# Optimization experiments

Hardware: AMD Instinct MI355X
Metric: run time of the kernel (lower is better)

## Reference

```python
import jax, jax.numpy as jnp
import numpy as np

SEQ_LEN, BATCH, INPUT, HIDDEN, OUTPUT = 2048, 64, 256, 256, 256


def setup_inputs() -> dict:
    key = jax.random.key(0)
    ks = jax.random.split(key, 6)
    return {
        "x": jax.random.normal(ks[0], (SEQ_LEN, BATCH, INPUT), dtype=jnp.float32),
        "h0": jax.random.normal(ks[1], (BATCH, HIDDEN), dtype=jnp.float32),
        "i2h_weight": jax.random.normal(ks[2], (INPUT + HIDDEN, HIDDEN), dtype=jnp.float32) * 0.05,
        "i2h_bias": jax.random.normal(ks[3], (HIDDEN,), dtype=jnp.float32) * 0.05,
        "h2o_weight": jax.random.normal(ks[4], (HIDDEN, OUTPUT), dtype=jnp.float32) * 0.05,
        "h2o_bias": jax.random.normal(ks[5], (OUTPUT,), dtype=jnp.float32) * 0.05,
    }


def reference(x, h0, i2h_weight, i2h_bias, h2o_weight, h2o_bias):
    # Vanilla RNN: per timestep t:
    #   h = tanh(concat(x_t, h) @ W_i2h + b_i2h)
    #   y_t = h @ W_h2o + b_h2o
    # Split W_i2h into input/hidden blocks so the concat is expressed as two GEMMs.
    w_xh = i2h_weight[:x.shape[-1]]   # [input, hidden]
    w_hh = i2h_weight[x.shape[-1]:]   # [hidden, hidden]

    def step(h, x_t):
        h_new = jnp.tanh(x_t @ w_xh + h @ w_hh + i2h_bias)  # [batch, hidden]
        y_t = h_new @ h2o_weight + h2o_bias                  # [batch, output]
        return h_new, y_t

    _, outputs = jax.lax.scan(step, h0, x)  # outputs: [seq, batch, output]
    return outputs
```

## Files before the change

### kernel.cpp

```cpp
#include <hip/hip_runtime.h>
#include <cstdint>
#include <cstddef>

typedef __attribute__((ext_vector_type(8))) short short8;
typedef __attribute__((ext_vector_type(4))) float f32x4;
typedef __attribute__((ext_vector_type(2))) float f32x2;
typedef __attribute__((ext_vector_type(2))) unsigned int u32x2;

#define SEQ 2048
#define NB  64
#define HID 256
#define M_TOTAL (SEQ*NB)

__device__ __forceinline__ unsigned short f2bf(float x){
  unsigned u = __float_as_uint(x);
  u += 0x7fffu + ((u>>16)&1u);
  return (unsigned short)(u>>16);
}

__global__ void k_convert_x(const float* __restrict__ x, unsigned short* __restrict__ xb){
  size_t i = (size_t)blockIdx.x*256 + threadIdx.x;
  f32x4 v = ((const f32x4*)x)[i];
  unsigned a0=f2bf(v[0]), a1=f2bf(v[1]), a2=f2bf(v[2]), a3=f2bf(v[3]);
  u32x2 o; o[0] = a0 | (a1<<16); o[1] = a2 | (a3<<16);
  ((u32x2*)xb)[i] = o;
}

__global__ void k_convert_w(const float* __restrict__ i2h, const float* __restrict__ h2o,
                            unsigned short* __restrict__ BT1, unsigned short* __restrict__ BT3){
  int k = blockIdx.x; int n = threadIdx.x;
  BT1[n*256+k] = f2bf(i2h[k*256+n]);
  BT3[n*256+k] = f2bf(h2o[k*256+n]);
}

__global__ __launch_bounds__(256) void k_gemm(
    const unsigned short* __restrict__ A, const unsigned short* __restrict__ BT,
    const float* __restrict__ bias, float* __restrict__ C)
{
  __shared__ __align__(16) unsigned short As[128*64];
  __shared__ __align__(16) unsigned short Bs[128*64];
  int tid = threadIdx.x;
  int bm = blockIdx.x, bn = blockIdx.y;
  int l = tid & 63, wv = tid >> 6;
  int wm = wv >> 1, wn = wv & 1;
  int lr = l & 15, lq = l >> 4;

  f32x4 acc[4][4];
  #pragma unroll
  for (int i=0;i<4;i++)
    #pragma unroll
    for (int j=0;j<4;j++) acc[i][j] = (f32x4)0.f;

  for (int kb=0; kb<4; ++kb){
    int k0 = kb*64;
    #pragma unroll
    for (int it=0; it<4; ++it){
      int f = it*256 + tid;
      int m = f >> 3;
      int kk = (f & 7) * 8;
      short8 va = *(const short8*)(A  + (size_t)(bm*128+m)*256 + k0 + kk);
      short8 vb = *(const short8*)(BT + (size_t)(bn*128+m)*256 + k0 + kk);
      *(short8*)(As + m*64 + kk) = va;
      *(short8*)(Bs + m*64 + kk) = vb;
    }
    __syncthreads();
    #pragma unroll
    for (int kt=0; kt<2; ++kt){
      short8 af[4], bfr[4];
      #pragma unroll
      for (int mt=0;mt<4;mt++){
        int row = wm*64 + mt*16 + lr;
        af[mt] = *(const short8*)(As + row*64 + kt*32 + lq*8);
      }
      #pragma unroll
      for (int nt=0;nt<4;nt++){
        int row = wn*64 + nt*16 + lr;
        bfr[nt] = *(const short8*)(Bs + row*64 + kt*32 + lq*8);
      }
      #pragma unroll
      for (int mt=0;mt<4;mt++)
        #pragma unroll
        for (int nt=0;nt<4;nt++)
          acc[mt][nt] = __builtin_amdgcn_mfma_f32_16x16x32_bf16(af[mt], bfr[nt], acc[mt][nt], 0, 0, 0);
    }
    __syncthreads();
  }
  #pragma unroll
  for (int nt=0;nt<4;nt++){
    int gn = bn*128 + wn*64 + nt*16 + lr;
    float bv = bias[gn];
    #pragma unroll
    for (int mt=0;mt<4;mt++){
      int gm = bm*128 + wm*64 + mt*16 + lq*4;
      #pragma unroll
      for (int r=0;r<4;r++)
        C[(size_t)(gm+r)*256 + gn] = acc[mt][nt][r] + bv;
    }
  }
}

__global__ __launch_bounds__(1024, 4) void k_scan(
    const float* __restrict__ i2h,
    const float* __restrict__ h0,
    const float* __restrict__ pre,
    unsigned short* __restrict__ H)
{
  __shared__ __align__(16) float hbuf[256];
  __shared__ __align__(16) float red[16*256];
  int b   = blockIdx.x;
  int tid = threadIdx.x;
  int jg  = tid & 63;
  int kc  = tid >> 6;

  f32x4 w[16];
  const float* Wp = i2h + (size_t)(256 + kc*16)*256 + jg*4;
  #pragma unroll
  for (int i=0;i<16;i++)
    w[i] = *(const f32x4*)(Wp + (size_t)i*256);

  if (tid < 256) hbuf[tid] = h0[b*256 + tid];

  float pv = 0.f, p1 = 0.f;
  if (tid < 256){
    pv = pre[(size_t)b*256 + tid];
    p1 = pre[((size_t)1*NB + b)*256 + tid];
  }
  __syncthreads();

  float* myred = red + kc*256 + jg*4;

  for (int t=0; t<SEQ; ++t){
    const f32x4* hp = (const f32x4*)(hbuf + kc*16);
    f32x4 acc = (f32x4)0.f;
    #pragma unroll
    for (int i=0;i<4;i++){
      f32x4 h4 = hp[i];
      acc += h4[0]*w[4*i+0];
      acc += h4[1]*w[4*i+1];
      acc += h4[2]*w[4*i+2];
      acc += h4[3]*w[4*i+3];
    }
    *(f32x4*)myred = acc;
    __syncthreads();

    if (tid < 256){
      float p2 = (t+2 < SEQ) ? pre[((size_t)(t+2)*NB + b)*256 + tid] : 0.f;
      float s = pv;
      #pragma unroll
      for (int k2=0;k2<16;k2++) s += red[k2*256 + tid];
      float e = __expf(2.f*s);
      float h = 1.f - 2.f/(e+1.f);
      hbuf[tid] = h;
      H[((size_t)t*NB + b)*256 + tid] = f2bf(h);
      pv = p1; p1 = p2;
    }
    __syncthreads();
  }
}

extern "C" void kernel_launch(void* const* d_in, const int* in_sizes, int n_in,
                              void* d_out, int out_size, void* d_ws, size_t ws_size,
                              hipStream_t stream) {
  const float* x     = (const float*)d_in[0];
  const float* h0    = (const float*)d_in[1];
  const float* i2h   = (const float*)d_in[2];
  const float* i2h_b = (const float*)d_in[3];
  const float* h2o   = (const float*)d_in[4];
  const float* h2o_b = (const float*)d_in[5];
  float* out = (float*)d_out;

  unsigned short* xb  = (unsigned short*)d_ws;
  unsigned short* BT1 = (unsigned short*)((char*)d_ws + (size_t)M_TOTAL*HID*2);
  unsigned short* BT3 = BT1 + 256*256;

  k_convert_x<<<M_TOTAL*HID/(256*4), 256, 0, stream>>>(x, xb);
  k_convert_w<<<256, 256, 0, stream>>>(i2h, h2o, BT1, BT3);

  dim3 g1(M_TOTAL/128, 2);
  k_gemm<<<g1, 256, 0, stream>>>(xb, BT1, i2h_b, out);
  k_scan<<<NB, 1024, 0, stream>>>(i2h, h0, out, xb);
  k_gemm<<<g1, 256, 0, stream>>>(xb, BT3, h2o_b, out);
}
```

Before: 1.654 ms.

## Reduce scan partial sums with DPP lane rotations and lighter barriers

New measurement: 1.965 ms. 18.8% more time.

```diff
diff --git a/kernel.cpp b/kernel.cpp
--- a/kernel.cpp
+++ b/kernel.cpp
@@ -16,6 +16,12 @@
   unsigned u = __float_as_uint(x);
   u += 0x7fffu + ((u>>16)&1u);
   return (unsigned short)(u>>16);
+}
+
+template<int CTRL>
+__device__ __forceinline__ float dpp_rot(float x){
+  return __int_as_float(__builtin_amdgcn_update_dpp(
+      0, __float_as_int(x), CTRL, 0xF, 0xF, true));
 }
 
 __global__ void k_convert_x(const float* __restrict__ x, unsigned short* __restrict__ xb){
@@ -106,55 +112,81 @@
     unsigned short* __restrict__ H)
 {
   __shared__ __align__(16) float hbuf[256];
-  __shared__ __align__(16) float red[16*256];
-  int b   = blockIdx.x;
-  int tid = threadIdx.x;
-  int jg  = tid & 63;
-  int kc  = tid >> 6;
-
-  f32x4 w[16];
-  const float* Wp = i2h + (size_t)(256 + kc*16)*256 + jg*4;
+  __shared__ __align__(16) float red[4*256];
+  const int b   = blockIdx.x;
+  const int tid = threadIdx.x;
+  const int l   = tid & 63;
+  const int wv  = tid >> 6;
+  const int ks  = wv & 3;
+  const int kc  = l & 3;
+  const int j0  = (wv >> 2)*64 + (l >> 2)*4;
+
+  f32x4 wr[16];
+  {
+    const float* Wb = i2h + (size_t)256*256 + ((size_t)(ks*64 + kc*16))*256 + j0;
+    #pragma unroll
+    for (int m=0;m<16;m++) wr[m] = *(const f32x4*)(Wb + (size_t)m*256);
+  }
   #pragma unroll
-  for (int i=0;i<16;i++)
-    w[i] = *(const f32x4*)(Wp + (size_t)i*256);
+  for (int m=0;m<16;m++) asm volatile("" : "+v"(wr[m]));
 
   if (tid < 256) hbuf[tid] = h0[b*256 + tid];
 
   float pv = 0.f, p1 = 0.f;
+  const float* prep = pre + (size_t)b*256 + tid;
+  unsigned short* Hp = H + (size_t)b*256 + tid;
   if (tid < 256){
-    pv = pre[(size_t)b*256 + tid];
-    p1 = pre[((size_t)1*NB + b)*256 + tid];
+    pv = prep[0];
+    p1 = prep[(size_t)NB*256];
+    prep += (size_t)2*NB*256;
   }
   __syncthreads();
 
-  float* myred = red + kc*256 + jg*4;
+  const f32x4* hv = (const f32x4*)hbuf + (ks*16 + kc*4);
+  float* redw = red + ks*256 + j0;
 
   for (int t=0; t<SEQ; ++t){
-    const f32x4* hp = (const f32x4*)(hbuf + kc*16);
-    f32x4 acc = (f32x4)0.f;
-    #pragma unroll
-    for (int i=0;i<4;i++){
-      f32x4 h4 = hp[i];
-      acc += h4[0]*w[4*i+0];
-      acc += h4[1]*w[4*i+1];
-      acc += h4[2]*w[4*i+2];
-      acc += h4[3]*w[4*i+3];
-    }
-    *(f32x4*)myred = acc;
-    __syncthreads();
+    f32x4 hA = hv[0], hB = hv[1], hC = hv[2], hD = hv[3];
+    f32x4 a0, a1;
+    a0  = hA[0]*wr[0];   a1  = hA[1]*wr[1];
+    a0 += hA[2]*wr[2];   a1 += hA[3]*wr[3];
+    a0 += hB[0]*wr[4];   a1 += hB[1]*wr[5];
+    a0 += hB[2]*wr[6];   a1 += hB[3]*wr[7];
+    a0 += hC[0]*wr[8];   a1 += hC[1]*wr[9];
+    a0 += hC[2]*wr[10];  a1 += hC[3]*wr[11];
+    a0 += hD[0]*wr[12];  a1 += hD[1]*wr[13];
+    a0 += hD[2]*wr[14];  a1 += hD[3]*wr[15];
+    f32x4 acc = a0 + a1;
+
+    #pragma unroll
+    for (int c=0;c<4;c++){
+      float v = acc[c];
+      v += dpp_rot<0x39>(v);
+      v += dpp_rot<0x4E>(v);
+      acc[c] = v;
+    }
+    if (kc == 0) *(f32x4*)redw = acc;
+
+    asm volatile("s_waitcnt lgkmcnt(0)" ::: "memory");
+    __builtin_amdgcn_s_barrier();
+    asm volatile("" ::: "memory");
 
     if (tid < 256){
-      float p2 = (t+2 < SEQ) ? pre[((size_t)(t+2)*NB + b)*256 + tid] : 0.f;
-      float s = pv;
-      #pragma unroll
-      for (int k2=0;k2<16;k2++) s += red[k2*256 + tid];
+      float p2 = 0.f;
+      if (t + 2 < SEQ) p2 = prep[0];
+      prep += (size_t)NB*256;
+      float s = pv + red[tid] + red[256+tid] + red[512+tid] + red[768+tid];
       float e = __expf(2.f*s);
-      float h = 1.f - 2.f/(e+1.f);
+      float h = 1.f - 2.f*__builtin_amdgcn_rcpf(e + 1.f);
       hbuf[tid] = h;
-      H[((size_t)t*NB + b)*256 + tid] = f2bf(h);
+      *Hp = f2bf(h);
+      Hp += (size_t)NB*256;
       pv = p1; p1 = p2;
     }
-    __syncthreads();
+
+    asm volatile("s_waitcnt lgkmcnt(0)" ::: "memory");
+    __builtin_amdgcn_s_barrier();
+    asm volatile("" ::: "memory");
   }
 }
 
```
